# Kernel optimization log

Hardware: AMD Instinct MI355X
Metric: run time of the kernel (lower is better)

## Reference

```python
import jax, jax.numpy as jnp
import numpy as np

DIM = 768
HEADS = 12
HEAD_DIM = DIM // HEADS
SCALE = HEAD_DIM ** -0.5


def setup_inputs() -> dict:
    key = jax.random.key(0)
    k1, k2, k3, k4 = jax.random.split(key, 4)
    x = jax.random.normal(k1, (1, 4096, DIM), dtype=jnp.float32)
    # qkv: Linear(dim, 3*dim), bias=False
    W_qkv = jax.random.normal(k2, (DIM, 3 * DIM), dtype=jnp.float32) * (DIM ** -0.5)
    # proj: Linear(dim, dim) with bias
    W_proj = jax.random.normal(k3, (DIM, DIM), dtype=jnp.float32) * (DIM ** -0.5)
    b_proj = jax.random.normal(k4, (DIM,), dtype=jnp.float32) * 0.01
    return {"x": x, "W_qkv": W_qkv, "W_proj": W_proj, "b_proj": b_proj}


def reference(x, W_qkv, W_proj, b_proj):
    b, n, d = x.shape
    qkv = x @ W_qkv                                  # [b, n, 3d]
    q, k, v = jnp.split(qkv, 3, axis=-1)             # each [b, n, d]
    # split heads: [b, n, (h hd)] -> [b, h, n, hd]
    def heads(t):
        return t.reshape(b, n, HEADS, HEAD_DIM).transpose(0, 2, 1, 3)
    q, k, v = heads(q) * SCALE, heads(k), heads(v)
    sim = jnp.einsum('bhid,bhjd->bhij', q, k)        # [b, h, n, n] -- full score matrix
    attn = jax.nn.softmax(sim, axis=-1)
    out = jnp.einsum('bhij,bhjd->bhid', attn, v)     # [b, h, n, hd]
    out = out.transpose(0, 2, 1, 3).reshape(b, n, d)  # merge heads
    return out @ W_proj + b_proj
```

## Files before the change

### kernel.cpp

```cpp
#include <hip/hip_runtime.h>
#include <math.h>

#define TOKENS 4096
#define DMODEL 768
#define NHEADS 12
#define HDIM   64
#define QKV_N  2304
#define ATTN_SCALE 0.125f
#define QSCALE_LOG2E (0.125f * 1.44269504088896340736f)

typedef __attribute__((ext_vector_type(8))) short bf16x8;
typedef __attribute__((ext_vector_type(4))) float floatx4;

__device__ __forceinline__ ushort f2bf(float f) {
    union { float f; unsigned u; } cv; cv.f = f;
    unsigned u = cv.u;
    u += 0x7fffu + ((u >> 16) & 1u);
    return (ushort)(u >> 16);
}

__device__ __forceinline__ unsigned cvt_pk_bf16(float a, float b) {
    unsigned r;
    asm("v_cvt_pk_bf16_f32 %0, %1, %2" : "=v"(r) : "v"(a), "v"(b));
    return r;
}

__device__ __forceinline__ void gl2lds16(const ushort* g, ushort* l) {
    __builtin_amdgcn_global_load_lds(
        (const __attribute__((address_space(1))) void*)g,
        (__attribute__((address_space(3))) void*)l, 16, 0, 0);
}

__device__ __forceinline__ bf16x8 frag(const ushort* ls, int row, int chunk) {
    return *(const bf16x8*)(ls + row * 64 + ((chunk ^ (row & 7)) * 8));
}

__global__ __launch_bounds__(256) void prep_kernel(
    const float* __restrict__ x, const float* __restrict__ Wqkv,
    const float* __restrict__ Wproj, ushort* __restrict__ Xb,
    ushort* __restrict__ WqkvT, ushort* __restrict__ WprojT)
{
    __shared__ ushort tile[32][33];
    const int bid = blockIdx.x;
    const int tid = threadIdx.x;

    if (bid < 3072) {
        const int i = bid * 256 + tid;
        const float4 v = ((const float4*)x)[i];
        ushort4 h;
        h.x = f2bf(v.x); h.y = f2bf(v.y); h.z = f2bf(v.z); h.w = f2bf(v.w);
        ((ushort4*)Xb)[i] = h;
        return;
    }

    const float* in; ushort* out; int C, bx, by;
    if (bid < 3072 + 1728) {
        const int b = bid - 3072;
        in = Wqkv; out = WqkvT; C = QKV_N;
        bx = b % 72; by = b / 72;
    } else {
        const int b = bid - 4800;
        in = Wproj; out = WprojT; C = DMODEL;
        bx = b % 24; by = b / 24;
    }
    const int R  = DMODEL;
    const int tx = tid & 31;
    const int ty8 = tid >> 5;
    const int c0 = bx * 32;
    const int r0 = by * 32;
    #pragma unroll
    for (int p = 0; p < 4; ++p) {
        const int r = ty8 + p * 8;
        tile[r][tx] = f2bf(in[(size_t)(r0 + r) * C + c0 + tx]);
    }
    __syncthreads();
    #pragma unroll
    for (int p = 0; p < 4; ++p) {
        const int c = ty8 + p * 8;
        out[(size_t)(c0 + c) * R + r0 + tx] = tile[tx][c];
    }
}

template<int NT>
__device__ __forceinline__ void gemm_body_2ph(
    const ushort* __restrict__ A, const ushort* __restrict__ Bt, int K,
    int m0, int n0, floatx4 acc[4][NT], ushort* ls)
{
    const int BUF = 8192 + 2048 * NT;

    const int tid  = threadIdx.x;
    const int lane = tid & 63;
    const int wave = tid >> 6;
    const int wm = wave >> 1, wn = wave & 1;
    const int quad = lane >> 4, l16 = lane & 15;

    const int lrow = lane >> 3;
    const int csw  = ((lane & 7) ^ lrow) * 8;

    const ushort* gA = A  + (size_t)(m0 + wave * 32 + lrow) * K + csw;
    const ushort* gB = Bt + (size_t)(n0 + wave * NT * 8 + lrow) * K + csw;
    const int lAoff = (wave * 32) * 64;
    const int lBoff = 8192 + (wave * NT * 8) * 64;

    #pragma unroll
    for (int p = 0; p < 4; ++p)
        gl2lds16(gA + (size_t)p * 8 * K, ls + lAoff + p * 8 * 64);
    #pragma unroll
    for (int p = 0; p < NT; ++p)
        gl2lds16(gB + (size_t)p * 8 * K, ls + lBoff + p * 8 * 64);
    __syncthreads();

    const int NK = K / 64;
    for (int t = 0; t < NK; ++t) {
        ushort* cb = ls + (t & 1) * BUF;
        ushort* nb = ls + ((t + 1) & 1) * BUF;

        if (t + 1 < NK) {
            const int k1 = (t + 1) * 64;
            #pragma unroll
            for (int p = 0; p < 4; ++p)
                gl2lds16(gA + (size_t)p * 8 * K + k1, nb + lAoff + p * 8 * 64);
            #pragma unroll
            for (int p = 0; p < NT; ++p)
                gl2lds16(gB + (size_t)p * 8 * K + k1, nb + lBoff + p * 8 * 64);
        }

        const ushort* lsA = cb;
        const ushort* lsB = cb + 8192;
        #pragma unroll
        for (int ks = 0; ks < 2; ++ks) {
            bf16x8 af[4], bfr[NT];
            #pragma unroll
            for (int mt = 0; mt < 4; ++mt)
                af[mt] = frag(lsA, wm * 64 + mt * 16 + l16, ks * 4 + quad);
            #pragma unroll
            for (int nt = 0; nt < NT; ++nt)
                bfr[nt] = frag(lsB, wn * NT * 16 + nt * 16 + l16, ks * 4 + quad);
            #pragma unroll
            for (int mt = 0; mt < 4; ++mt)
                #pragma unroll
                for (int nt = 0; nt < NT; ++nt)
                    acc[mt][nt] = __builtin_amdgcn_mfma_f32_16x16x32_bf16(
                        af[mt], bfr[nt], acc[mt][nt], 0, 0, 0);
        }

        __syncthreads();
    }
}

__global__ __launch_bounds__(256) void gemm_qkv_mfma(
    const ushort* __restrict__ Xb, const ushort* __restrict__ Wt,
    ushort* __restrict__ Qb, ushort* __restrict__ Kb, ushort* __restrict__ Vt)
{
    __shared__ __align__(16) ushort ls[32768];
    const int lin = blockIdx.x + blockIdx.y * 18;
    const int w   = (lin & 7) * 72 + (lin >> 3);
    const int m0  = (w / 18) * 128;
    const int n0  = (w % 18) * 128;

    floatx4 acc[4][4] = {};
    gemm_body_2ph<4>(Xb, Wt, DMODEL, m0, n0, acc, ls);

    const int tid  = threadIdx.x;
    const int lane = tid & 63;
    const int wave = tid >> 6;
    const int wm = wave >> 1, wn = wave & 1;
    const int quad = lane >> 4, l16 = lane & 15;

    if (n0 < 2 * DMODEL) {
        const float scale = (n0 < DMODEL) ? QSCALE_LOG2E : 1.0f;
        ushort* outp = (n0 < DMODEL) ? Qb : Kb;
        const int colg = (n0 < DMODEL) ? n0 : n0 - DMODEL;
        __syncthreads();
        #pragma unroll
        for (int mt = 0; mt < 4; ++mt)
            #pragma unroll
            for (int nt = 0; nt < 4; ++nt) {
                const int row = wm * 64 + mt * 16 + quad * 4;
                const int col = wn * 64 + nt * 16 + l16;
                #pragma unroll
                for (int r = 0; r < 4; ++r)
                    ls[(row + r) * 136 + col] = f2bf(acc[mt][nt][r] * scale);
            }
        __syncthreads();
        #pragma unroll
        for (int p2 = 0; p2 < 8; ++p2) {
            const int row = (tid >> 4) + p2 * 16;
            const int c8  = (tid & 15) * 8;
            *(uint4*)(outp + (size_t)(m0 + row) * DMODEL + colg + c8) =
                *(const uint4*)(ls + row * 136 + c8);
        }
    } else {
        const int hd0 = n0 - 2 * DMODEL;
        __syncthreads();
        #pragma unroll
        for (int mt = 0; mt < 4; ++mt)
            #pragma unroll
            for (int nt = 0; nt < 4; ++nt) {
                const int hd  = wn * 64 + nt * 16 + l16;
                const int tok = wm * 64 + mt * 16 + quad * 4;
                #pragma unroll
                for (int r = 0; r < 4; ++r)
                    ls[hd * 136 + tok + r] = f2bf(acc[mt][nt][r]);
            }
        __syncthreads();
        #pragma unroll
        for (int p2 = 0; p2 < 8; ++p2) {
            const int row = (tid >> 4) + p2 * 16;
            const int c8  = (tid & 15) * 8;
            *(uint4*)(Vt + (size_t)(hd0 + row) * TOKENS + m0 + c8) =
                *(const uint4*)(ls + row * 136 + c8);
        }
    }
}

__global__ __launch_bounds__(256) void gemm_proj_mfma(
    const ushort* __restrict__ Ab, const ushort* __restrict__ Wt,
    const float* __restrict__ bias, float* __restrict__ out)
{
    __shared__ __align__(16) ushort ls[24576];
    const int lin = blockIdx.x + blockIdx.y * 12;
    const int w   = (lin & 7) * 48 + (lin >> 3);
    const int m0  = (w / 12) * 128;
    const int n0  = (w % 12) * 64;

    floatx4 acc[4][2] = {};
    gemm_body_2ph<2>(Ab, Wt, DMODEL, m0, n0, acc, ls);

    const int lane = threadIdx.x & 63;
    const int wave = threadIdx.x >> 6;
    const int wm = wave >> 1, wn = wave & 1;
    const int quad = lane >> 4, l16 = lane & 15;
    const int row0 = m0 + wm * 64 + quad * 4;
    const int col0 = n0 + wn * 32;

    #pragma unroll
    for (int nt = 0; nt < 2; ++nt) {
        const int col = col0 + nt * 16 + l16;
        const float bv = bias[col];
        #pragma unroll
        for (int mt = 0; mt < 4; ++mt)
            #pragma unroll
            for (int r = 0; r < 4; ++r)
                out[(size_t)(row0 + mt * 16 + r) * DMODEL + col] =
                    acc[mt][nt][r] + bv;
    }
}

__global__ __launch_bounds__(256, 3) void attn_mfma_kernel(
    const ushort* __restrict__ Qb, const ushort* __restrict__ Kb,
    const ushort* __restrict__ Vt, ushort* __restrict__ attn_out)
{
    __shared__ __align__(16) ushort lds[25728];

    const int tid  = threadIdx.x;
    const int wave = tid >> 6;
    const int lane = tid & 63;
    const int quad = lane >> 4;
    const int l16  = lane & 15;

    const int lin = blockIdx.x + blockIdx.y * 64;
    const int wsw = (lin & 7) * 96 + (lin >> 3);
    const int h   = wsw >> 6;
    const int i0  = (wsw & 63) * 64;

    bf16x8 qf[4][2];
    #pragma unroll
    for (int jt = 0; jt < 4; ++jt) {
        const ushort* qb = Qb + (size_t)(i0 + jt * 16 + l16) * DMODEL + h * HDIM;
        qf[jt][0] = *(const bf16x8*)(qb + quad * 8);
        qf[jt][1] = *(const bf16x8*)(qb + 32 + quad * 8);
    }

    bf16x8 ones;
    #pragma unroll
    for (int i = 0; i < 8; ++i) ones[i] = (short)0x3F80;

    floatx4 O[4][4] = {};
    floatx4 Ol[4]   = {};

    ushort* wls = lds + wave * 6144;

    const int lrow8 = lane >> 3;
    const int csw8  = ((lane & 7) ^ lrow8) * 8;
    const ushort* gK0 = Kb + (size_t)(wave * 16 + lrow8) * DMODEL + h * HDIM + csw8;
    const ushort* gK1 = gK0 + (size_t)8 * DMODEL;

    const ushort* gV0 = Vt + (size_t)(h * HDIM + (lane >> 1)) * TOKENS
                           + wave * 16 + (((lane & 1) ^ ((lane >> 3) & 1)) * 8);
    const ushort* gV1 = gV0 + (size_t)32 * TOKENS;

    const int vo = ((quad >> 1) ^ ((l16 >> 2) & 1)) * 8 + (quad & 1) * 4;

    union { bf16x8 v; unsigned u[4]; } pa[4];

    gl2lds16(gK0, wls);
    gl2lds16(gK1, wls + 512);
    gl2lds16(gV0, wls + 2048);
    gl2lds16(gV1, wls + 2048 + 512);

    for (int u = 0; u < 32; ++u) {
        const int s0 = (u & 1) << 1;
        ushort* Kc0 = wls;
        ushort* Kc1 = wls + 1024;
        ushort* V0  = wls + 2048 + s0 * 1024;
        ushort* V1  = wls + 2048 + (s0 + 1) * 1024;
        ushort* Vn  = wls + 2048 + ((s0 + 2) & 3) * 1024;

        {
            const size_t t1 = (size_t)(2 * u + 1) * 64;
            gl2lds16(gK0 + t1 * DMODEL, Kc1);
            gl2lds16(gK1 + t1 * DMODEL, Kc1 + 512);
            gl2lds16(gV0 + t1, V1);
            gl2lds16(gV1 + t1, V1 + 512);
        }
        asm volatile("s_waitcnt vmcnt(4)" ::: "memory");

        {
            const bf16x8 a0 = frag(Kc0, l16, quad);
            const bf16x8 a1 = frag(Kc0, l16, 4 + quad);
            __builtin_amdgcn_s_setprio(1);
            #pragma unroll
            for (int jt = 0; jt < 4; ++jt) {
                floatx4 s = {0.f, 0.f, 0.f, 0.f};
                s = __builtin_amdgcn_mfma_f32_16x16x32_bf16(a0, qf[jt][0], s, 0, 0, 0);
                s = __builtin_amdgcn_mfma_f32_16x16x32_bf16(a1, qf[jt][1], s, 0, 0, 0);
                pa[jt].u[0] = cvt_pk_bf16(__builtin_amdgcn_exp2f(s[0]),
                                          __builtin_amdgcn_exp2f(s[1]));
                pa[jt].u[1] = cvt_pk_bf16(__builtin_amdgcn_exp2f(s[2]),
                                          __builtin_amdgcn_exp2f(s[3]));
            }
            __builtin_amdgcn_s_setprio(0);
        }

        if (u < 31) {
            const size_t t2 = (size_t)(2 * u + 2) * 64;
            gl2lds16(gK0 + t2 * DMODEL, Kc0);
            gl2lds16(gK1 + t2 * DMODEL, Kc0 + 512);
            gl2lds16(gV0 + t2, Vn);
            gl2lds16(gV1 + t2, Vn + 512);
            asm volatile("s_waitcnt vmcnt(4)" ::: "memory");
        } else {
            asm volatile("s_waitcnt vmcnt(0)" ::: "memory");
        }

        {
            const bf16x8 a0 = frag(Kc1, l16, quad);
            const bf16x8 a1 = frag(Kc1, l16, 4 + quad);
            __builtin_amdgcn_s_setprio(1);
            #pragma unroll
            for (int jt = 0; jt < 4; ++jt) {
                floatx4 s = {0.f, 0.f, 0.f, 0.f};
                s = __builtin_amdgcn_mfma_f32_16x16x32_bf16(a0, qf[jt][0], s, 0, 0, 0);
                s = __builtin_amdgcn_mfma_f32_16x16x32_bf16(a1, qf[jt][1], s, 0, 0, 0);
                pa[jt].u[2] = cvt_pk_bf16(__builtin_amdgcn_exp2f(s[0]),
                                          __builtin_amdgcn_exp2f(s[1]));
                pa[jt].u[3] = cvt_pk_bf16(__builtin_amdgcn_exp2f(s[2]),
                                          __builtin_amdgcn_exp2f(s[3]));
            }
            __builtin_amdgcn_s_setprio(0);
        }

        __builtin_amdgcn_s_setprio(1);
        #pragma unroll
        for (int nt = 0; nt < 4; ++nt) {
            const int ro = (nt * 16 + l16) * 16 + vo;
            union { bf16x8 v; uint2 d[2]; } vu;
            vu.d[0] = *(const uint2*)(V0 + ro);
            vu.d[1] = *(const uint2*)(V1 + ro);
            #pragma unroll
            for (int jt = 0; jt < 4; ++jt)
                O[jt][nt] = __builtin_amdgcn_mfma_f32_16x16x32_bf16(
                    pa[jt].v, vu.v, O[jt][nt], 0, 0, 0);
        }
        #pragma unroll
        for (int jt = 0; jt < 4; ++jt)
            Ol[jt] = __builtin_amdgcn_mfma_f32_16x16x32_bf16(
                pa[jt].v, ones, Ol[jt], 0, 0, 0);
        __builtin_amdgcn_s_setprio(0);
    }

    __syncthreads();
    float* Of  = (float*)lds;
    float* Olf = ((float*)lds) + 3 * 64 * 66;
    if (wave != 0) {
        const int rg = (wave - 1) * 64 * 66;
        #pragma unroll
        for (int jt = 0; jt < 4; ++jt) {
            #pragma unroll
            for (int nt = 0; nt < 4; ++nt)
                #pragma unroll
                for (int r = 0; r < 4; ++r)
                    Of[rg + (jt * 16 + quad * 4 + r) * 66 + nt * 16 + l16] = O[jt][nt][r];
            if (l16 == 0) {
                #pragma unroll
                for (int r = 0; r < 4; ++r)
                    Olf[(wave - 1) * 64 + jt * 16 + quad * 4 + r] = Ol[jt][r];
            }
        }
    }
    __syncthreads();
    if (wave == 0) {
        #pragma unroll
        for (int jt = 0; jt < 4; ++jt) {
            const int qr = jt * 16 + quad * 4;
            float linv[4];
            #pragma unroll
            for (int r = 0; r < 4; ++r) {
                const float l = Ol[jt][r] + Olf[qr + r] + Olf[64 + qr + r]
                              + Olf[128 + qr + r];
                linv[r] = __builtin_amdgcn_rcpf(l);
            }
            #pragma unroll
            for (int nt = 0; nt < 4; ++nt) {
                const int d = h * HDIM + nt * 16 + l16;
                #pragma unroll
                for (int r = 0; r < 4; ++r) {
                    const float o = O[jt][nt][r]
                        + Of[(qr + r) * 66 + nt * 16 + l16]
                        + Of[64 * 66 + (qr + r) * 66 + nt * 16 + l16]
                        + Of[2 * 64 * 66 + (qr + r) * 66 + nt * 16 + l16];
                    attn_out[(size_t)(i0 + qr + r) * DMODEL + d] = f2bf(o * linv[r]);
                }
            }
        }
    }
}

extern "C" void kernel_launch(void* const* d_in, const int* in_sizes, int n_in,
                              void* d_out, int out_size, void* d_ws, size_t ws_size,
                              hipStream_t stream)
{
    const float* x     = (const float*)d_in[0];
    const float* Wqkv  = (const float*)d_in[1];
    const float* Wproj = (const float*)d_in[2];
    const float* bproj = (const float*)d_in[3];
    float* out = (float*)d_out;

    ushort* Xb     = (ushort*)d_ws;
    ushort* WqkvT  = Xb    + (size_t)TOKENS * DMODEL;
    ushort* WprojT = WqkvT + (size_t)QKV_N * DMODEL;
    ushort* Qb     = WprojT + (size_t)DMODEL * DMODEL;
    ushort* Kb     = Qb    + (size_t)TOKENS * DMODEL;
    ushort* Vt     = Kb    + (size_t)TOKENS * DMODEL;
    ushort* attn   = Vt    + (size_t)TOKENS * DMODEL;

    prep_kernel<<<dim3(5376), 256, 0, stream>>>(
        x, Wqkv, Wproj, Xb, WqkvT, WprojT);

    gemm_qkv_mfma<<<dim3(QKV_N / 128, TOKENS / 128), 256, 0, stream>>>(
        Xb, WqkvT, Qb, Kb, Vt);

    attn_mfma_kernel<<<dim3(TOKENS / 64, NHEADS), 256, 0, stream>>>(
        Qb, Kb, Vt, attn);

    gemm_proj_mfma<<<dim3(DMODEL / 64, TOKENS / 128), 256, 0, stream>>>(
        attn, WprojT, bproj, out);
}
```

Before: 181.4 us.

## Enlarge QKV GEMM tile to 128x256 with 512-thread blocks and double-buffered K loop

The QKV projection GEMM now uses 128x256 output tiles computed by 8 waves (2x4) in 512-thread blocks, launched as 288 blocks in a 1D grid with a swizzled tile order. Its K loop is inlined with double-buffered async global-to-LDS loads and XOR-swizzled columns. The aim is more operand reuse per block and more overlap of loads with MFMA work. In exchange the kernel uses more LDS, runs one block per CU, and has fewer blocks to spread across the CUs.

```diff
diff --git a/kernel.cpp b/kernel.cpp
--- a/kernel.cpp
+++ b/kernel.cpp
@@ -148,57 +148,111 @@
     }
 }
 
-__global__ __launch_bounds__(256) void gemm_qkv_mfma(
+__global__ __launch_bounds__(512, 1) void gemm_qkv_mfma(
     const ushort* __restrict__ Xb, const ushort* __restrict__ Wt,
     ushort* __restrict__ Qb, ushort* __restrict__ Kb, ushort* __restrict__ Vt)
 {
-    __shared__ __align__(16) ushort ls[32768];
-    const int lin = blockIdx.x + blockIdx.y * 18;
-    const int w   = (lin & 7) * 72 + (lin >> 3);
-    const int m0  = (w / 18) * 128;
-    const int n0  = (w % 18) * 128;
-
-    floatx4 acc[4][4] = {};
-    gemm_body_2ph<4>(Xb, Wt, DMODEL, m0, n0, acc, ls);
+    __shared__ __align__(16) ushort ls[49152];
+
+    const int lin = blockIdx.x;
+    const int w   = (lin & 7) * 36 + (lin >> 3);
+    const int m0  = (w / 9) * 128;
+    const int n0  = (w % 9) * 256;
+    const int K   = DMODEL;
 
     const int tid  = threadIdx.x;
     const int lane = tid & 63;
     const int wave = tid >> 6;
-    const int wm = wave >> 1, wn = wave & 1;
+    const int wm2  = wave >> 2;
+    const int wn4  = wave & 3;
     const int quad = lane >> 4, l16 = lane & 15;
+
+    const int lrow = lane >> 3;
+    const int csw  = ((lane & 7) ^ lrow) * 8;
+
+    const ushort* gA = Xb + (size_t)(m0 + wave * 16 + lrow) * K + csw;
+    const ushort* gB = Wt + (size_t)(n0 + wave * 32 + lrow) * K + csw;
+    const int lAoff = (wave * 16) * 64;
+    const int lBoff = 8192 + (wave * 32) * 64;
+    const int BUF = 24576;
+
+    floatx4 acc[4][4] = {};
+
+    #pragma unroll
+    for (int p = 0; p < 2; ++p)
+        gl2lds16(gA + (size_t)p * 8 * K, ls + lAoff + p * 8 * 64);
+    #pragma unroll
+    for (int p = 0; p < 4; ++p)
+        gl2lds16(gB + (size_t)p * 8 * K, ls + lBoff + p * 8 * 64);
+    __syncthreads();
+
+    const int NK = K / 64;
+    for (int t = 0; t < NK; ++t) {
+        ushort* cb = ls + (t & 1) * BUF;
+        ushort* nb = ls + ((t + 1) & 1) * BUF;
+
+        if (t + 1 < NK) {
+            const int k1 = (t + 1) * 64;
+            #pragma unroll
+            for (int p = 0; p < 2; ++p)
+                gl2lds16(gA + (size_t)p * 8 * K + k1, nb + lAoff + p * 8 * 64);
+            #pragma unroll
+            for (int p = 0; p < 4; ++p)
+                gl2lds16(gB + (size_t)p * 8 * K + k1, nb + lBoff + p * 8 * 64);
+        }
+
+        const ushort* lsA = cb;
+        const ushort* lsB = cb + 8192;
+        #pragma unroll
+        for (int ks = 0; ks < 2; ++ks) {
+            bf16x8 af[4], bfr[4];
+            #pragma unroll
+            for (int mt = 0; mt < 4; ++mt)
+                af[mt] = frag(lsA, wm2 * 64 + mt * 16 + l16, ks * 4 + quad);
+            #pragma unroll
+            for (int nt = 0; nt < 4; ++nt)
+                bfr[nt] = frag(lsB, wn4 * 64 + nt * 16 + l16, ks * 4 + quad);
+            #pragma unroll
+            for (int mt = 0; mt < 4; ++mt)
+                #pragma unroll
+                for (int nt = 0; nt < 4; ++nt)
+                    acc[mt][nt] = __builtin_amdgcn_mfma_f32_16x16x32_bf16(
+                        af[mt], bfr[nt], acc[mt][nt], 0, 0, 0);
+        }
+
+        __syncthreads();
+    }
 
     if (n0 < 2 * DMODEL) {
         const float scale = (n0 < DMODEL) ? QSCALE_LOG2E : 1.0f;
         ushort* outp = (n0 < DMODEL) ? Qb : Kb;
         const int colg = (n0 < DMODEL) ? n0 : n0 - DMODEL;
+        #pragma unroll
+        for (int mt = 0; mt < 4; ++mt)
+            #pragma unroll
+            for (int nt = 0; nt < 4; ++nt) {
+                const int row = wm2 * 64 + mt * 16 + quad * 4;
+                const int col = wn4 * 64 + nt * 16 + l16;
+                #pragma unroll
+                for (int r = 0; r < 4; ++r)
+                    ls[(row + r) * 264 + col] = f2bf(acc[mt][nt][r] * scale);
+            }
         __syncthreads();
         #pragma unroll
-        for (int mt = 0; mt < 4; ++mt)
-            #pragma unroll
-            for (int nt = 0; nt < 4; ++nt) {
-                const int row = wm * 64 + mt * 16 + quad * 4;
-                const int col = wn * 64 + nt * 16 + l16;
-                #pragma unroll
-                for (int r = 0; r < 4; ++r)
-                    ls[(row + r) * 136 + col] = f2bf(acc[mt][nt][r] * scale);
-            }
-        __syncthreads();
-        #pragma unroll
         for (int p2 = 0; p2 < 8; ++p2) {
-            const int row = (tid >> 4) + p2 * 16;
-            const int c8  = (tid & 15) * 8;
-            *(uint4*)(outp + (size_t)(m0 + row) * DMODEL + colg + c8) =
-                *(const uint4*)(ls + row * 136 + c8);
+            const int row = (tid >> 5) + p2 * 16;
+            const int c16 = (tid & 31) * 8;
+            *(uint4*)(outp + (size_t)(m0 + row) * DMODEL + colg + c16) =
+                *(const uint4*)(ls + row * 264 + c16);
         }
     } else {
         const int hd0 = n0 - 2 * DMODEL;
-        __syncthreads();
         #pragma unroll
         for (int mt = 0; mt < 4; ++mt)
             #pragma unroll
             for (int nt = 0; nt < 4; ++nt) {
-                const int hd  = wn * 64 + nt * 16 + l16;
-                const int tok = wm * 64 + mt * 16 + quad * 4;
+                const int hd  = wn4 * 64 + nt * 16 + l16;
+                const int tok = wm2 * 64 + mt * 16 + quad * 4;
                 #pragma unroll
                 for (int r = 0; r < 4; ++r)
                     ls[hd * 136 + tok + r] = f2bf(acc[mt][nt][r]);
@@ -206,7 +260,7 @@
         __syncthreads();
         #pragma unroll
         for (int p2 = 0; p2 < 8; ++p2) {
-            const int row = (tid >> 4) + p2 * 16;
+            const int row = (tid >> 4) + p2 * 32;
             const int c8  = (tid & 15) * 8;
             *(uint4*)(Vt + (size_t)(hd0 + row) * TOKENS + m0 + c8) =
                 *(const uint4*)(ls + row * 136 + c8);
@@ -448,7 +502,7 @@
     prep_kernel<<<dim3(5376), 256, 0, stream>>>(
         x, Wqkv, Wproj, Xb, WqkvT, WprojT);
 
-    gemm_qkv_mfma<<<dim3(QKV_N / 128, TOKENS / 128), 256, 0, stream>>>(
+    gemm_qkv_mfma<<<dim3(288), 512, 0, stream>>>(
         Xb, WqkvT, Qb, Kb, Vt);
 
     attn_mfma_kernel<<<dim3(TOKENS / 64, NHEADS), 256, 0, stream>>>(
```

Result: no change. 180.2 us (-0.7%).

## Use K=32 double-buffered tiles in QKV GEMM to cut LDS and raise occupancy

Applied to the files above, without the earlier changes.

Adds a GEMM body variant that stages 32-wide K slices, with its own swizzle, into double-buffered LDS. This shrinks the QKV GEMM shared allocation from 64KB to about 34KB and adds a launch bound of 3 blocks per CU. The aim is more resident blocks to hide global-load latency. In exchange it runs twice as many K iterations, each with a barrier and less MFMA work to overlap the loads.

```diff
diff --git a/kernel.cpp b/kernel.cpp
--- a/kernel.cpp
+++ b/kernel.cpp
@@ -33,6 +33,10 @@
 
 __device__ __forceinline__ bf16x8 frag(const ushort* ls, int row, int chunk) {
     return *(const bf16x8*)(ls + row * 64 + ((chunk ^ (row & 7)) * 8));
+}
+
+__device__ __forceinline__ bf16x8 frag32(const ushort* ls, int row, int chunk) {
+    return *(const bf16x8*)(ls + row * 32 + ((chunk ^ (row & 3)) * 8));
 }
 
 __global__ __launch_bounds__(256) void prep_kernel(
@@ -148,18 +152,82 @@
     }
 }
 
-__global__ __launch_bounds__(256) void gemm_qkv_mfma(
+template<int NT>
+__device__ __forceinline__ void gemm_body_2ph32(
+    const ushort* __restrict__ A, const ushort* __restrict__ Bt, int K,
+    int m0, int n0, floatx4 acc[4][NT], ushort* ls)
+{
+    const int BUF = 4096 + 1024 * NT;
+
+    const int tid  = threadIdx.x;
+    const int lane = tid & 63;
+    const int wave = tid >> 6;
+    const int wm = wave >> 1, wn = wave & 1;
+    const int quad = lane >> 4, l16 = lane & 15;
+
+    const int lrow = lane >> 2;
+    const int csw  = ((lane & 3) ^ (lrow & 3)) * 8;
+
+    const ushort* gA = A  + (size_t)(m0 + wave * 32 + lrow) * K + csw;
+    const ushort* gB = Bt + (size_t)(n0 + wave * NT * 8 + lrow) * K + csw;
+    const int lAoff = wave * 1024;
+    const int lBoff = 4096 + wave * NT * 256;
+
+    #pragma unroll
+    for (int p = 0; p < 2; ++p)
+        gl2lds16(gA + (size_t)p * 16 * K, ls + lAoff + p * 512);
+    #pragma unroll
+    for (int p = 0; p < NT / 2; ++p)
+        gl2lds16(gB + (size_t)p * 16 * K, ls + lBoff + p * 512);
+    __syncthreads();
+
+    const int NK = K / 32;
+    for (int t = 0; t < NK; ++t) {
+        ushort* cb = ls + (t & 1) * BUF;
+        ushort* nb = ls + ((t + 1) & 1) * BUF;
+
+        if (t + 1 < NK) {
+            const int k1 = (t + 1) * 32;
+            #pragma unroll
+            for (int p = 0; p < 2; ++p)
+                gl2lds16(gA + (size_t)p * 16 * K + k1, nb + lAoff + p * 512);
+            #pragma unroll
+            for (int p = 0; p < NT / 2; ++p)
+                gl2lds16(gB + (size_t)p * 16 * K + k1, nb + lBoff + p * 512);
+        }
+
+        const ushort* lsA = cb;
+        const ushort* lsB = cb + 4096;
+        bf16x8 af[4], bfr[NT];
+        #pragma unroll
+        for (int mt = 0; mt < 4; ++mt)
+            af[mt] = frag32(lsA, wm * 64 + mt * 16 + l16, quad);
+        #pragma unroll
+        for (int nt = 0; nt < NT; ++nt)
+            bfr[nt] = frag32(lsB, wn * NT * 16 + nt * 16 + l16, quad);
+        #pragma unroll
+        for (int mt = 0; mt < 4; ++mt)
+            #pragma unroll
+            for (int nt = 0; nt < NT; ++nt)
+                acc[mt][nt] = __builtin_amdgcn_mfma_f32_16x16x32_bf16(
+                    af[mt], bfr[nt], acc[mt][nt], 0, 0, 0);
+
+        __syncthreads();
+    }
+}
+
+__global__ __launch_bounds__(256, 3) void gemm_qkv_mfma(
     const ushort* __restrict__ Xb, const ushort* __restrict__ Wt,
     ushort* __restrict__ Qb, ushort* __restrict__ Kb, ushort* __restrict__ Vt)
 {
-    __shared__ __align__(16) ushort ls[32768];
+    __shared__ __align__(16) ushort ls[17408];
     const int lin = blockIdx.x + blockIdx.y * 18;
     const int w   = (lin & 7) * 72 + (lin >> 3);
     const int m0  = (w / 18) * 128;
     const int n0  = (w % 18) * 128;
 
     floatx4 acc[4][4] = {};
-    gemm_body_2ph<4>(Xb, Wt, DMODEL, m0, n0, acc, ls);
+    gemm_body_2ph32<4>(Xb, Wt, DMODEL, m0, n0, acc, ls);
 
     const int tid  = threadIdx.x;
     const int lane = tid & 63;
```

New measurement: 176.6 us. -2.6%, faster.
